# Performance work log

Measured on AMD Instinct MI355X. Metric: run time of the kernel, lower is better.

## Reference

```python
import jax, jax.numpy as jnp
import numpy as np

PATCH = 3
PAD = PATCH // 2  # stride = 1


def _extract_patches(x):
    """torch F.unfold(k=3, s=1, p=1) reshaped to [b, n=h*w, c*3*3] (c slowest, then ki, kj)."""
    b, c, h, w = x.shape
    xp = jnp.pad(x, ((0, 0), (0, 0), (PAD, PAD), (PAD, PAD)))
    # stack the 9 shifted views -> [b, c, 9, h, w]
    pats = jnp.stack([xp[:, :, i:i + h, j:j + w]
                      for i in range(PATCH) for j in range(PATCH)], axis=2)
    pats = pats.reshape(b, c, PATCH, PATCH, h, w)
    # -> [b, h*w, c*PATCH*PATCH], matching torch unfold channel ordering
    return pats.transpose(0, 4, 5, 1, 2, 3).reshape(b, h * w, c * PATCH * PATCH)


def _l2_normalize(x):
    # F.normalize(dim=2): x / max(||x||_2, 1e-12)
    n = jnp.linalg.norm(x, axis=2, keepdims=True)
    return x / jnp.maximum(n, 1e-12)


def _fold(patches_flat, c, h, w):
    """torch F.fold(k=3, s=1, p=1): overlap-add patches back to [b, c, h, w]."""
    b = patches_flat.shape[0]
    p = patches_flat.reshape(b, h, w, c, PATCH, PATCH)
    out = jnp.zeros((b, c, h + 2 * PAD, w + 2 * PAD), patches_flat.dtype)
    for i in range(PATCH):
        for j in range(PATCH):
            out = out.at[:, :, i:i + h, j:j + w].add(
                p[:, :, :, :, i, j].transpose(0, 3, 1, 2))
    return out[:, :, PAD:PAD + h, PAD:PAD + w]


def setup_inputs() -> dict:
    key = jax.random.key(0)
    k1, k2 = jax.random.split(key)
    B, C, H, W = 1, 256, 96, 96
    return {
        "content_features": jax.random.normal(k1, (B, C, H, W), dtype=jnp.float32),
        "style_features": jax.random.normal(k2, (B, C, H, W), dtype=jnp.float32),
    }


def reference(content_features, style_features):
    b, c, h, w = content_features.shape
    cpat = _extract_patches(content_features)   # [b, n, d]
    spat = _extract_patches(style_features)     # [b, m, d]
    # all-pairs cosine similarity: [b, n, m]
    sim = jnp.einsum('bnd,bmd->bnm', _l2_normalize(cpat), _l2_normalize(spat))
    best = jnp.argmax(sim, axis=2)              # [b, n]
    matched = jnp.take_along_axis(spat, best[:, :, None], axis=1)  # [b, n, d]
    num = _fold(matched, c, h, w)
    den = _fold(jnp.ones_like(matched), c, h, w)
    return num / (den + 1e-8)
```

## Files before the change

### kernel.cpp

```cpp
#include <hip/hip_runtime.h>

#define HH 96
#define WW 96
#define CCH 256
#define NPIX (HH*WW)
#define HP 98
#define NROWS 9604
#define CORE_LO 99
#define CORE_HI 9505
#define CAND_CAP 256

typedef unsigned short u16;
typedef _Float16 f16;
typedef _Float16 f16x8 __attribute__((ext_vector_type(8)));
typedef float f32x4 __attribute__((ext_vector_type(4)));

__device__ __forceinline__ f32x4 ld4u(const float* p) {
    f32x4 r; __builtin_memcpy(&r, p, 16); return r;
}
__device__ __forceinline__ float dec_key(unsigned ku) {
    return (ku & 0x80000000u) ? __uint_as_float(ku ^ 0x80000000u)
                              : __uint_as_float(~ku);
}
__device__ __forceinline__ unsigned enc_key(float v) {
    unsigned u = __float_as_uint(v);
    return (u & 0x80000000u) ? ~u : (u | 0x80000000u);
}
__device__ __forceinline__ int pad2m(int mp) {
    int yq = mp / HP, xq = mp - yq * HP;
    return (yq - 1) * WW + (xq - 1);
}

__device__ __forceinline__ void stage4(const u16* const* srcs, u16* dst, int kb) {
#pragma unroll
    for (int t = 0; t < 4; ++t)
        __builtin_amdgcn_global_load_lds(
            (const __attribute__((address_space(1))) unsigned int*)(srcs[t] + kb),
            (__attribute__((address_space(3))) unsigned int*)(dst + t * 512),
            16, 0, 0);
}

__global__ __launch_bounds__(256) void xsth_kernel(const float* __restrict__ X,
                                                   float* __restrict__ XT,
                                                   u16* __restrict__ XTh) {
    __shared__ float tile[64][65];
    const int p0 = blockIdx.x * 64, c0 = blockIdx.y * 64;
    const int rr = threadIdx.x >> 6, cl = threadIdx.x & 63;
#pragma unroll
    for (int r = 0; r < 16; ++r)
        tile[rr * 16 + r][cl] = X[(c0 + rr * 16 + r) * NPIX + p0 + cl];
    __syncthreads();
#pragma unroll
    for (int r = 0; r < 16; ++r) {
        float v = tile[cl][rr * 16 + r];
        long long o = (long long)(p0 + rr * 16 + r) * CCH + c0 + cl;
        XT[o] = v;
        f16 h = (f16)v;
        u16 hb; __builtin_memcpy(&hb, &h, 2);
        XTh[o] = hb;
    }
}

__global__ __launch_bounds__(256) void prep_kernel(const float* __restrict__ X,
                                                   float* __restrict__ ssum,
                                                   unsigned long long* __restrict__ keys,
                                                   int* __restrict__ cnt,
                                                   unsigned* __restrict__ dropMax,
                                                   int reset) {
    int p = blockIdx.x * 256 + threadIdx.x;
    if (p >= NPIX) return;
    float s = 0.f;
#pragma unroll 8
    for (int c = 0; c < CCH; ++c) {
        float v = X[c * NPIX + p];
        s = fmaf(v, v, s);
    }
    ssum[p] = s;
    if (reset) { keys[p] = 0ULL; cnt[p] = 0; dropMax[p] = 0u; }
}

__global__ __launch_bounds__(256) void rnsbp_kernel(const float* __restrict__ ssum,
                                                    float* __restrict__ rnsp,
                                                    float* __restrict__ biasp) {
    int mp = blockIdx.x * 256 + threadIdx.x;
    if (mp >= 9632) return;
    int yq = mp / HP, xq = mp - yq * HP;
    bool real = (yq >= 1 && yq <= 96 && xq >= 1 && xq <= 96);
    if (!real) { rnsp[mp] = 0.f; biasp[mp] = -3e38f; return; }
    int y = yq - 1, x = xq - 1;
    float s = 0.f;
    for (int dy = -1; dy <= 1; ++dy) {
        int yy = y + dy;
        if ((unsigned)yy >= HH) continue;
        for (int dx = -1; dx <= 1; ++dx) {
            int xx = x + dx;
            if ((unsigned)xx >= WW) continue;
            s += ssum[yy * WW + xx];
        }
    }
    rnsp[mp] = 1.f / fmaxf(sqrtf(s), 1e-12f);
    biasp[mp] = 0.f;
}

__global__ __launch_bounds__(256) void cthr_kernel(const float* __restrict__ ssum,
                                                   float* __restrict__ thr) {
    int n = blockIdx.x * 256 + threadIdx.x;
    if (n >= NPIX) return;
    int y = n / WW, x = n - y * WW;
    float s = 0.f;
    for (int dy = -1; dy <= 1; ++dy) {
        int yy = y + dy;
        if ((unsigned)yy >= HH) continue;
        for (int dx = -1; dx <= 1; ++dx) {
            int xx = x + dx;
            if ((unsigned)xx >= WW) continue;
            s += ssum[yy * WW + xx];
        }
    }
    thr[n] = 0.0036f * sqrtf(s);
}

__global__ __launch_bounds__(256) void padzero_kernel(float* __restrict__ cc, int wstride) {
    int p = blockIdx.x;
    int yq = p / HP, xq = p - yq * HP;
    if (yq >= 1 && yq <= 96 && xq >= 1 && xq <= 96) return;
    const f32x4 z = {0.f, 0.f, 0.f, 0.f};
    float* row = cc + (long long)p * wstride;
    for (int c = threadIdx.x * 4; c < wstride; c += 1024)
        *(f32x4*)&row[c] = z;
}

__global__ __launch_bounds__(256, 4) void cc_gemm_kernel(
        const u16* __restrict__ ChT, const u16* __restrict__ ShT,
        const u16* __restrict__ zbuf,
        float* __restrict__ cc, int csp, int wstride) {
    __shared__ u16 lds[2][2][8][64][8];

    const int tid = threadIdx.x;
    const int n0 = blockIdx.x * 128;
    const int m0 = blockIdx.y * 128;
    const int wave = tid >> 6, lane = tid & 63;
    const int wr = wave >> 1, wc = wave & 1;
    const int rlo = lane & 15, kseg = (lane >> 4) * 8;
    const int isB = wave >> 1;
    const int tb = (wave & 1) * 4;

    const u16* srcs[4];
    if (!isB) {
#pragma unroll
        for (int t = 0; t < 4; ++t)
            srcs[t] = ChT + (n0 + (tb + t) * 16 + rlo) * CCH + kseg;
    } else {
#pragma unroll
        for (int t = 0; t < 4; ++t) {
            int qp = csp + m0 + (tb + t) * 16 + rlo;
            int yq = qp / HP, xq = qp - yq * HP;
            bool ok = (qp < NROWS) && (yq >= 1 && yq <= 96 && xq >= 1 && xq <= 96);
            srcs[t] = ok ? (ShT + ((yq - 1) * WW + (xq - 1)) * CCH + kseg)
                         : (zbuf + kseg);
        }
    }
    u16* slab0 = &lds[0][isB][tb][0][0];
    u16* slab1 = &lds[1][isB][tb][0][0];

    f32x4 acc[4][4];
#pragma unroll
    for (int i = 0; i < 4; ++i)
#pragma unroll
        for (int j = 0; j < 4; ++j) acc[i][j] = (f32x4){0.f, 0.f, 0.f, 0.f};

    stage4(srcs, slab0, 0);
    stage4(srcs, slab1, 32);

#define READS(CUR)                                                          \
    f16x8 ah[4], bh[4];                                                     \
    _Pragma("unroll")                                                       \
    for (int i = 0; i < 4; ++i) {                                           \
        ah[i] = *(const f16x8*)&lds[CUR][0][wr * 4 + i][lane][0];           \
        bh[i] = *(const f16x8*)&lds[CUR][1][wc * 4 + i][lane][0];           \
    }

#define MFMAS                                                               \
    _Pragma("unroll")                                                       \
    for (int i = 0; i < 4; ++i)                                             \
        _Pragma("unroll")                                                   \
        for (int j = 0; j < 4; ++j)                                         \
            acc[i][j] = __builtin_amdgcn_mfma_f32_16x16x32_f16(ah[i], bh[j], acc[i][j], 0, 0, 0);

#define KSTEP(KK, WN)                                                       \
    {                                                                       \
        asm volatile("s_waitcnt vmcnt(" #WN ")" ::: "memory");              \
        __builtin_amdgcn_sched_barrier(0);                                  \
        __builtin_amdgcn_s_barrier();                                       \
        READS((KK) & 1)                                                     \
        asm volatile("s_waitcnt lgkmcnt(0)" ::: "memory");                  \
        __builtin_amdgcn_sched_barrier(0);                                  \
        __builtin_amdgcn_s_barrier();                                       \
        if ((KK) + 2 < 8)                                                   \
            stage4(srcs, (((KK) & 1)) ? slab1 : slab0, ((KK) + 2) * 32);    \
        __builtin_amdgcn_sched_barrier(0);                                  \
        MFMAS                                                               \
    }

    KSTEP(0, 4) KSTEP(1, 4) KSTEP(2, 4) KSTEP(3, 4)
    KSTEP(4, 4) KSTEP(5, 4) KSTEP(6, 4) KSTEP(7, 0)

#undef KSTEP
#undef MFMAS
#undef READS

    const int r0 = (lane >> 4) * 4;
    const int cl = lane & 15;
#pragma unroll
    for (int i = 0; i < 4; ++i) {
        const int prow = n0 + wr * 64 + i * 16 + r0;
#pragma unroll
        for (int r = 0; r < 4; ++r) {
            const int row = prow + r;
            const int pp = row + 2 * (row / WW) + CORE_LO;
            const long long base = (long long)pp * wstride + m0 + wc * 64 + cl;
#pragma unroll
            for (int j = 0; j < 4; ++j)
                cc[base + j * 16] = acc[i][j][r];
        }
    }
}

__global__ __launch_bounds__(256) void boxsum_kernel(
        const float* __restrict__ cc, const float* __restrict__ rnsp,
        const float* __restrict__ biasp, const float* __restrict__ thr,
        unsigned long long* __restrict__ keys,
        int* __restrict__ cnt, float* __restrict__ candV, u16* __restrict__ candI,
        unsigned* __restrict__ dropMax,
        int core0, int coreEnd, int csp, int wstride) {
    const int wave = threadIdx.x >> 6, lane = threadIdx.x & 63;
    const int n = blockIdx.x * 4 + wave;
    const int pp = n + 2 * (n / WW) + CORE_LO;
    const long long rowbase = (long long)pp * wstride - csp;
    const int W1 = wstride + 1;
    const float thrn = thr[n];

    float wprior = -1e30f;
    {
        unsigned long long k0 = keys[n];
        if (k0) wprior = dec_key((unsigned)(k0 >> 32));
    }

    const int OFF[9] = {-99, -98, -97, -1, 0, 1, 97, 98, 99};
    const float* tp[9];
#pragma unroll
    for (int t = 0; t < 9; ++t)
        tp[t] = cc + rowbase + core0 + lane * 4 + (long long)OFF[t] * W1;

    float v1 = -3e38f, v2 = -3e38f;
    int i1 = 0;
    for (int mq = core0 + lane * 4; mq < coreEnd; mq += 256) {
        f32x4 s = {0.f, 0.f, 0.f, 0.f};
#pragma unroll
        for (int t = 0; t < 9; ++t) { s += ld4u(tp[t]); tp[t] += 256; }
        f32x4 rv = ld4u(rnsp + mq);
        f32x4 bv = ld4u(biasp + mq);
#pragma unroll
        for (int sl = 0; sl < 4; ++sl) {
            float v = fmaf(s[sl], rv[sl], bv[sl]);
            if (mq + sl >= coreEnd) v = -3e38f;
            if (v > v1) { v2 = v1; v1 = v; i1 = mq + sl; }
            else if (v > v2) v2 = v;
        }
    }

    float wmax = v1;
#pragma unroll
    for (int d = 32; d; d >>= 1) wmax = fmaxf(wmax, __shfl_xor(wmax, d));
    wmax = fmaxf(wmax, wprior);
    const float lim = wmax - thrn;

    if (v1 >= lim) {
        int idx = atomicAdd(&cnt[n], 1);
        if (idx < CAND_CAP) {
            candV[n * CAND_CAP + idx] = v1;
            candI[n * CAND_CAP + idx] = (u16)pad2m(i1);
        } else {
            atomicMax(&dropMax[n], enc_key(v1));
        }
    }
    if (v2 >= lim) {
        const float* rp[9];
#pragma unroll
        for (int t = 0; t < 9; ++t)
            rp[t] = cc + rowbase + core0 + lane * 4 + (long long)OFF[t] * W1;
        for (int mq = core0 + lane * 4; mq < coreEnd; mq += 256) {
            f32x4 s = {0.f, 0.f, 0.f, 0.f};
#pragma unroll
            for (int t = 0; t < 9; ++t) { s += ld4u(rp[t]); rp[t] += 256; }
            f32x4 rv = ld4u(rnsp + mq);
            f32x4 bv = ld4u(biasp + mq);
#pragma unroll
            for (int sl = 0; sl < 4; ++sl) {
                float v = fmaf(s[sl], rv[sl], bv[sl]);
                if (mq + sl < coreEnd && v >= lim && (mq + sl) != i1) {
                    int idx = atomicAdd(&cnt[n], 1);
                    if (idx < CAND_CAP) {
                        candV[n * CAND_CAP + idx] = v;
                        candI[n * CAND_CAP + idx] = (u16)pad2m(mq + sl);
                    } else {
                        atomicMax(&dropMax[n], enc_key(v));
                    }
                }
            }
        }
    }
    if (lane == 0)
        atomicMax(&keys[n], ((unsigned long long)enc_key(wmax)) << 32);
}

__global__ __launch_bounds__(256) void rescore_kernel(
        const float* __restrict__ XcT, const float* __restrict__ XsT,
        const float* __restrict__ rnsp, const float* __restrict__ thr,
        const unsigned long long* __restrict__ keys,
        const int* __restrict__ cnt, const float* __restrict__ candV,
        const u16* __restrict__ candI, const unsigned* __restrict__ dropMax,
        int* __restrict__ bestm) {
    const int wave = threadIdx.x >> 6, lane = threadIdx.x & 63;
    const int n = blockIdx.x * 4 + wave;
    int c = cnt[n]; if (c > CAND_CAP) c = CAND_CAP;
    const float M = dec_key((unsigned)(keys[n] >> 32));
    const float lim = M - thr[n];

    unsigned dm = dropMax[n];
    bool fallback = dm && (dec_key(dm) >= lim);
    if (!fallback) {
        int npass = 0, lastk = -1;
        for (int k = 0; k < c; ++k) {
            if (candV[n * CAND_CAP + k] >= lim) { ++npass; if (lastk < 0) lastk = k; }
        }
        if (npass == 1) {
            if (lane == 0) bestm[n] = candI[n * CAND_CAP + lastk];
            return;
        }
    }

    const int yn = n / WW, xn = n - yn * WW;
    const f32x4 z = {0.f, 0.f, 0.f, 0.f};
    f32x4 an[9];
#pragma unroll
    for (int t = 0; t < 9; ++t) {
        int di = t / 3 - 1, dj = t % 3 - 1;
        bool ok = ((unsigned)(yn + di) < HH) && ((unsigned)(xn + dj) < WW);
        an[t] = ok ? ld4u(XcT + (long long)((yn + di) * WW + xn + dj) * CCH + lane * 4) : z;
    }
    float bv = -1e30f; int bm = 0x7fffffff;
    if (fallback) {
        for (int m = 0; m < NPIX; ++m) {
            int ym = m / WW, xm = m - ym * WW;
            f32x4 acc = z;
#pragma unroll
            for (int t = 0; t < 9; ++t) {
                int di = t / 3 - 1, dj = t % 3 - 1;
                if (((unsigned)(ym + di) < HH) && ((unsigned)(xm + dj) < WW))
                    acc += an[t] * ld4u(XsT + (long long)((ym + di) * WW + xm + dj) * CCH + lane * 4);
            }
            float d = acc[0] + acc[1] + acc[2] + acc[3];
#pragma unroll
            for (int dd = 32; dd; dd >>= 1) d += __shfl_xor(d, dd);
            float v = d * rnsp[(ym + 1) * HP + (xm + 1)];
            if (v > bv) { bv = v; bm = m; }
        }
    } else {
        for (int k = 0; k < c; ++k) {
            if (candV[n * CAND_CAP + k] < lim) continue;
            int m = candI[n * CAND_CAP + k];
            int ym = m / WW, xm = m - ym * WW;
            f32x4 acc = z;
#pragma unroll
            for (int t = 0; t < 9; ++t) {
                int di = t / 3 - 1, dj = t % 3 - 1;
                if (((unsigned)(ym + di) < HH) && ((unsigned)(xm + dj) < WW))
                    acc += an[t] * ld4u(XsT + (long long)((ym + di) * WW + xm + dj) * CCH + lane * 4);
            }
            float d = acc[0] + acc[1] + acc[2] + acc[3];
#pragma unroll
            for (int dd = 32; dd; dd >>= 1) d += __shfl_xor(d, dd);
            float v = d * rnsp[(ym + 1) * HP + (xm + 1)];
            if (v > bv || (v == bv && m < bm)) { bv = v; bm = m; }
        }
    }
    if (lane == 0) bestm[n] = bm;
}

__global__ __launch_bounds__(256) void fold2_kernel(const float* __restrict__ XsT,
                                                    const int* __restrict__ bestm,
                                                    float* __restrict__ outT) {
    const int wave = threadIdx.x >> 6, lane = threadIdx.x & 63;
    const int p = blockIdx.x * 4 + wave;
    const int y = p / WW, x = p - y * WW;
    f32x4 num = {0.f, 0.f, 0.f, 0.f};
    int den = 0;
#pragma unroll
    for (int i = 0; i < 3; ++i) {
        int ny = y + 1 - i;
        if ((unsigned)ny >= HH) continue;
#pragma unroll
        for (int j = 0; j < 3; ++j) {
            int nx = x + 1 - j;
            if ((unsigned)nx >= WW) continue;
            den++;
            int mg = bestm[ny * WW + nx];
            int my = mg / WW, mx = mg - my * WW;
            int sy = my + i - 1, sx = mx + j - 1;
            if ((unsigned)sy < HH && (unsigned)sx < WW)
                num += ld4u(XsT + (long long)(sy * WW + sx) * CCH + lane * 4);
        }
    }
    float inv = 1.f / ((float)den + 1e-8f);
    f32x4 o = {num[0] * inv, num[1] * inv, num[2] * inv, num[3] * inv};
    *(f32x4*)&outT[(long long)p * CCH + lane * 4] = o;
}

__global__ __launch_bounds__(256) void outtr_kernel(const float* __restrict__ outT,
                                                    float* __restrict__ out) {
    __shared__ float tile[64][65];
    const int p0 = blockIdx.x * 64, c0 = blockIdx.y * 64;
    const int t = threadIdx.x;
    const int rr = t >> 6, cl = t & 63;
#pragma unroll
    for (int r = 0; r < 16; ++r)
        tile[rr * 16 + r][cl] = outT[(long long)(p0 + rr * 16 + r) * CCH + c0 + cl];
    __syncthreads();
#pragma unroll
    for (int r = 0; r < 16; ++r)
        out[(long long)(c0 + rr * 16 + r) * NPIX + p0 + cl] = tile[cl][rr * 16 + r];
}

extern "C" void kernel_launch(void* const* d_in, const int* in_sizes, int n_in,
                              void* d_out, int out_size, void* d_ws, size_t ws_size,
                              hipStream_t stream) {
    (void)in_sizes; (void)n_in; (void)out_size;
    const float* Xc = (const float*)d_in[0];
    const float* Xs = (const float*)d_in[1];
    float* out = (float*)d_out;

    char* w = (char*)d_ws;
    unsigned long long* keys = (unsigned long long*)w;  w += (size_t)NPIX * 8;
    float* XcT  = (float*)w;                            w += (size_t)NPIX * CCH * 4;
    float* XsT  = (float*)w;                            w += (size_t)NPIX * CCH * 4;
    float* outT = (float*)w;                            w += (size_t)NPIX * CCH * 4;
    u16* XcH = (u16*)w;                                 w += (size_t)NPIX * CCH * 2;
    u16* XsH = (u16*)w;                                 w += (size_t)NPIX * CCH * 2;
    float* ssum_s = (float*)w;                          w += (size_t)NPIX * 4;
    float* ssum_c = (float*)w;                          w += (size_t)NPIX * 4;
    float* rnsp  = (float*)w;                           w += (size_t)9632 * 4;
    float* biasp = (float*)w;                           w += (size_t)9632 * 4;
    float* thr   = (float*)w;                           w += (size_t)NPIX * 4;
    int*   cnt   = (int*)w;                             w += (size_t)NPIX * 4;
    int*   bestm = (int*)w;                             w += (size_t)NPIX * 4;
    unsigned* dropMax = (unsigned*)w;                   w += (size_t)NPIX * 4;
    float* candV = (float*)w;                           w += (size_t)NPIX * CAND_CAP * 4;
    u16*   candI = (u16*)w;                             w += (size_t)NPIX * CAND_CAP * 2;
    u16*   zbuf  = (u16*)w;                             w += 1024;
    float* ccbuf = (float*)w;
    const size_t fixed = (size_t)(w - (char*)d_ws);

    long long avail = (ws_size > fixed + 4096)
                        ? (long long)(ws_size - fixed - 4096) : 0;
    int wstride = (int)(((avail / ((long long)NROWS * 4)) / 128) * 128);
    if (wstride > 2560) wstride = 2560;
    if (wstride < 512) wstride = 512;
    const int McCore = wstride - 198;

    hipMemsetAsync(zbuf, 0, 1024, stream);
    dim3 gt(NPIX / 64, CCH / 64);
    xsth_kernel<<<gt, 256, 0, stream>>>(Xc, XcT, XcH);
    xsth_kernel<<<gt, 256, 0, stream>>>(Xs, XsT, XsH);
    prep_kernel<<<NPIX / 256, 256, 0, stream>>>(Xs, ssum_s, keys, cnt, dropMax, 1);
    prep_kernel<<<NPIX / 256, 256, 0, stream>>>(Xc, ssum_c, keys, cnt, dropMax, 0);
    rnsbp_kernel<<<38, 256, 0, stream>>>(ssum_s, rnsp, biasp);
    cthr_kernel<<<NPIX / 256, 256, 0, stream>>>(ssum_c, thr);
    padzero_kernel<<<NROWS, 256, 0, stream>>>(ccbuf, wstride);

    for (int core0 = CORE_LO; core0 < CORE_HI; core0 += McCore) {
        int coreEnd = (core0 + McCore < CORE_HI) ? core0 + McCore : CORE_HI;
        int csp = core0 - 99;
        int ce = coreEnd + 99; if (ce > NROWS) ce = NROWS;
        int Wc = ce - csp;
        dim3 g(NPIX / 128, (Wc + 127) / 128);
        cc_gemm_kernel<<<g, 256, 0, stream>>>(XcH, XsH, zbuf, ccbuf, csp, wstride);
        boxsum_kernel<<<NPIX / 4, 256, 0, stream>>>(ccbuf, rnsp, biasp, thr,
                                                    keys, cnt, candV, candI, dropMax,
                                                    core0, coreEnd, csp, wstride);
    }

    rescore_kernel<<<NPIX / 4, 256, 0, stream>>>(XcT, XsT, rnsp, thr, keys,
                                                 cnt, candV, candI, dropMax, bestm);
    fold2_kernel<<<NPIX / 4, 256, 0, stream>>>(XsT, bestm, outT);
    outtr_kernel<<<gt, 256, 0, stream>>>(outT, out);
}
```

Before: 416.5 us.

## Process four consecutive content rows per wave in boxsum to reuse diagonal loads

Each wave now handles four consecutive content pixels instead of one. The 3x3 diagonal box-sum is reorganised so that each loaded row segment of the correlation buffer is shared across up to three neighbouring outputs. This cuts global loads from 36 to 18 rows, roughly 24 vector loads per iteration. The cost is more registers per thread (4x4 sums plus per-row top-2 state) and four times fewer blocks, which may lower occupancy. It also relies on the four pixels lying in the same image row, which holds because the row width of 96 is divisible by 4.

Measured after the change: 537.5 us. 1.29x slower.

```diff
diff --git a/kernel.cpp b/kernel.cpp
--- a/kernel.cpp
+++ b/kernel.cpp
@@ -234,84 +234,130 @@
         unsigned* __restrict__ dropMax,
         int core0, int coreEnd, int csp, int wstride) {
     const int wave = threadIdx.x >> 6, lane = threadIdx.x & 63;
-    const int n = blockIdx.x * 4 + wave;
-    const int pp = n + 2 * (n / WW) + CORE_LO;
-    const long long rowbase = (long long)pp * wstride - csp;
-    const int W1 = wstride + 1;
-    const float thrn = thr[n];
-
-    float wprior = -1e30f;
-    {
-        unsigned long long k0 = keys[n];
-        if (k0) wprior = dec_key((unsigned)(k0 >> 32));
-    }
-
-    const int OFF[9] = {-99, -98, -97, -1, 0, 1, 97, 98, 99};
-    const float* tp[9];
-#pragma unroll
-    for (int t = 0; t < 9; ++t)
-        tp[t] = cc + rowbase + core0 + lane * 4 + (long long)OFF[t] * W1;
-
-    float v1 = -3e38f, v2 = -3e38f;
-    int i1 = 0;
+    const int n0g = blockIdx.x * 16 + wave * 4;
+    const int pp0 = n0g + 2 * (n0g / WW) + CORE_LO;
+    const long long colbase = (long long)(core0 + lane * 4 - csp);
+
+    const float* pa[18];
+#pragma unroll
+    for (int grp = 0; grp < 3; ++grp) {
+        const int gb = (grp == 0) ? -99 : ((grp == 1) ? -1 : 97);
+#pragma unroll
+        for (int j = 0; j < 6; ++j) {
+            const int omin_rel = (j > 3) ? (j - 3) : 0;
+            pa[grp * 6 + j] = cc + (long long)(pp0 + gb + j) * wstride
+                                 + colbase + gb + omin_rel;
+        }
+    }
+
+    float v1[4], v2[4];
+    int i1[4];
+#pragma unroll
+    for (int g = 0; g < 4; ++g) { v1[g] = -3e38f; v2[g] = -3e38f; i1[g] = 0; }
+
     for (int mq = core0 + lane * 4; mq < coreEnd; mq += 256) {
-        f32x4 s = {0.f, 0.f, 0.f, 0.f};
-#pragma unroll
-        for (int t = 0; t < 9; ++t) { s += ld4u(tp[t]); tp[t] += 256; }
+        float s[4][4];
+#pragma unroll
+        for (int g = 0; g < 4; ++g)
+#pragma unroll
+            for (int sl = 0; sl < 4; ++sl) s[g][sl] = 0.f;
+
+#pragma unroll
+        for (int grp = 0; grp < 3; ++grp) {
+#pragma unroll
+            for (int j = 0; j < 6; ++j) {
+                const int k = grp * 6 + j;
+                const int omin_rel = (j > 3) ? (j - 3) : 0;
+                const int omax_rel = (j < 2) ? j : 2;
+                const int nd = omax_rel - omin_rel;
+                const int jj = (j > 3) ? 3 : j;
+                float w8[8];
+                f32x4 wa = ld4u(pa[k]);
+                w8[0] = wa[0]; w8[1] = wa[1]; w8[2] = wa[2]; w8[3] = wa[3];
+                if (nd > 0) {
+                    f32x4 wb = ld4u(pa[k] + 4);
+                    w8[4] = wb[0]; w8[5] = wb[1]; w8[6] = wb[2]; w8[7] = wb[3];
+                }
+#pragma unroll
+                for (int d = 0; d <= nd; ++d) {
+                    const int g = jj - d;
+#pragma unroll
+                    for (int sl = 0; sl < 4; ++sl)
+                        s[g][sl] += w8[d + sl];
+                }
+                pa[k] += 256;
+            }
+        }
         f32x4 rv = ld4u(rnsp + mq);
         f32x4 bv = ld4u(biasp + mq);
 #pragma unroll
         for (int sl = 0; sl < 4; ++sl) {
-            float v = fmaf(s[sl], rv[sl], bv[sl]);
-            if (mq + sl >= coreEnd) v = -3e38f;
-            if (v > v1) { v2 = v1; v1 = v; i1 = mq + sl; }
-            else if (v > v2) v2 = v;
-        }
-    }
-
-    float wmax = v1;
-#pragma unroll
-    for (int d = 32; d; d >>= 1) wmax = fmaxf(wmax, __shfl_xor(wmax, d));
-    wmax = fmaxf(wmax, wprior);
-    const float lim = wmax - thrn;
-
-    if (v1 >= lim) {
-        int idx = atomicAdd(&cnt[n], 1);
-        if (idx < CAND_CAP) {
-            candV[n * CAND_CAP + idx] = v1;
-            candI[n * CAND_CAP + idx] = (u16)pad2m(i1);
-        } else {
-            atomicMax(&dropMax[n], enc_key(v1));
-        }
-    }
-    if (v2 >= lim) {
-        const float* rp[9];
-#pragma unroll
-        for (int t = 0; t < 9; ++t)
-            rp[t] = cc + rowbase + core0 + lane * 4 + (long long)OFF[t] * W1;
-        for (int mq = core0 + lane * 4; mq < coreEnd; mq += 256) {
-            f32x4 s = {0.f, 0.f, 0.f, 0.f};
-#pragma unroll
-            for (int t = 0; t < 9; ++t) { s += ld4u(rp[t]); rp[t] += 256; }
-            f32x4 rv = ld4u(rnsp + mq);
-            f32x4 bv = ld4u(biasp + mq);
-#pragma unroll
-            for (int sl = 0; sl < 4; ++sl) {
-                float v = fmaf(s[sl], rv[sl], bv[sl]);
-                if (mq + sl < coreEnd && v >= lim && (mq + sl) != i1) {
-                    int idx = atomicAdd(&cnt[n], 1);
-                    if (idx < CAND_CAP) {
-                        candV[n * CAND_CAP + idx] = v;
-                        candI[n * CAND_CAP + idx] = (u16)pad2m(mq + sl);
-                    } else {
-                        atomicMax(&dropMax[n], enc_key(v));
+            const bool oob = (mq + sl >= coreEnd);
+#pragma unroll
+            for (int g = 0; g < 4; ++g) {
+                float v = fmaf(s[g][sl], rv[sl], bv[sl]);
+                if (oob) v = -3e38f;
+                if (v > v1[g]) { v2[g] = v1[g]; v1[g] = v; i1[g] = mq + sl; }
+                else if (v > v2[g]) v2[g] = v;
+            }
+        }
+    }
+
+#pragma unroll
+    for (int g = 0; g < 4; ++g) {
+        const int n = n0g + g;
+        const float thrn = thr[n];
+        float wprior = -1e30f;
+        {
+            unsigned long long k0 = keys[n];
+            if (k0) wprior = dec_key((unsigned)(k0 >> 32));
+        }
+        float wmax = v1[g];
+#pragma unroll
+        for (int d = 32; d; d >>= 1) wmax = fmaxf(wmax, __shfl_xor(wmax, d));
+        wmax = fmaxf(wmax, wprior);
+        const float lim = wmax - thrn;
+
+        if (v1[g] >= lim) {
+            int idx = atomicAdd(&cnt[n], 1);
+            if (idx < CAND_CAP) {
+                candV[n * CAND_CAP + idx] = v1[g];
+                candI[n * CAND_CAP + idx] = (u16)pad2m(i1[g]);
+            } else {
+                atomicMax(&dropMax[n], enc_key(v1[g]));
+            }
+        }
+        if (v2[g] >= lim) {
+            const int OFF[9] = {-99, -98, -97, -1, 0, 1, 97, 98, 99};
+            const long long rb = (long long)(pp0 + g) * wstride + colbase;
+            const float* rp[9];
+#pragma unroll
+            for (int t = 0; t < 9; ++t)
+                rp[t] = cc + rb + (long long)OFF[t] * (wstride + 1);
+            for (int mq = core0 + lane * 4; mq < coreEnd; mq += 256) {
+                f32x4 ss = {0.f, 0.f, 0.f, 0.f};
+#pragma unroll
+                for (int t = 0; t < 9; ++t) { ss += ld4u(rp[t]); rp[t] += 256; }
+                f32x4 rv = ld4u(rnsp + mq);
+                f32x4 bv = ld4u(biasp + mq);
+#pragma unroll
+                for (int sl = 0; sl < 4; ++sl) {
+                    float v = fmaf(ss[sl], rv[sl], bv[sl]);
+                    if (mq + sl < coreEnd && v >= lim && (mq + sl) != i1[g]) {
+                        int idx = atomicAdd(&cnt[n], 1);
+                        if (idx < CAND_CAP) {
+                            candV[n * CAND_CAP + idx] = v;
+                            candI[n * CAND_CAP + idx] = (u16)pad2m(mq + sl);
+                        } else {
+                            atomicMax(&dropMax[n], enc_key(v));
+                        }
                     }
                 }
             }
         }
-    }
-    if (lane == 0)
-        atomicMax(&keys[n], ((unsigned long long)enc_key(wmax)) << 32);
+        if (lane == 0)
+            atomicMax(&keys[n], ((unsigned long long)enc_key(wmax)) << 32);
+    }
 }
 
 __global__ __launch_bounds__(256) void rescore_kernel(
@@ -485,9 +531,9 @@
         int Wc = ce - csp;
         dim3 g(NPIX / 128, (Wc + 127) / 128);
         cc_gemm_kernel<<<g, 256, 0, stream>>>(XcH, XsH, zbuf, ccbuf, csp, wstride);
-        boxsum_kernel<<<NPIX / 4, 256, 0, stream>>>(ccbuf, rnsp, biasp, thr,
-                                                    keys, cnt, candV, candI, dropMax,
-                                                    core0, coreEnd, csp, wstride);
+        boxsum_kernel<<<NPIX / 16, 256, 0, stream>>>(ccbuf, rnsp, biasp, thr,
+                                                     keys, cnt, candV, candI, dropMax,
+                                                     core0, coreEnd, csp, wstride);
     }
 
     rescore_kernel<<<NPIX / 4, 256, 0, stream>>>(XcT, XsT, rnsp, thr, keys,
```
